# Optimization experiments

Measured on AMD Instinct MI355X. Metric: run time of the kernel, lower is better.

The kernel has to match this reference:

```python
import jax, jax.numpy as jnp
import numpy as np

INPUT_SIZE = 608
STRIDE = 32
NUM_CLASSES = 20
NMS_THRESH = 0.5
NUM_ANCHOR = 5
ANCHORS = np.array([[1.19, 1.98], [2.79, 4.59], [4.53, 8.92], [8.06, 5.29], [10.32, 10.65]], dtype=np.float32)


def _conv(x, w, b, pad):
    # x: NCHW, w: OIHW
    y = jax.lax.conv_general_dilated(x, w, (1, 1), [(pad, pad), (pad, pad)],
                                     dimension_numbers=('NCHW', 'OIHW', 'NCHW'))
    return y + b[None, :, None, None]


def _leaky(x):
    return jnp.where(x > 0, x, 0.1 * x)


def _reorg(x, s=2):
    # space-to-depth, darknet reorg: [B,C,H,W] -> [B,C*s*s,H/s,W/s]
    B, C, H, W = x.shape
    x = x.reshape(B, C, H // s, s, W // s, s)
    x = x.transpose(0, 3, 5, 1, 2, 4)
    return x.reshape(B, C * s * s, H // s, W // s)


def _forward_boxes_scores(feat_layer2, feat_layer3, w1a, b1a, w1b, b1b, wr, br, w2, b2, wp, bp):
    p5 = _leaky(_conv(feat_layer3, w1a, b1a, 1))
    p5 = _leaky(_conv(p5, w1b, b1b, 1))
    p4 = _reorg(_leaky(_conv(feat_layer2, wr, br, 0)))         # [1,256,19,19]
    p5 = jnp.concatenate([p4, p5], axis=1)                      # [1,1280,19,19]
    p5 = _leaky(_conv(p5, w2, b2, 1))
    pred = _conv(p5, wp, bp, 0)                                 # [1,125,19,19]
    B, C, H, W = pred.shape
    pred = pred.transpose(0, 2, 3, 1).reshape(B, H * W, C)
    conf = pred[:, :, :NUM_ANCHOR].reshape(B, H * W * NUM_ANCHOR, 1)
    cls = pred[:, :, NUM_ANCHOR:(1 + NUM_CLASSES) * NUM_ANCHOR].reshape(B, H * W * NUM_ANCHOR, NUM_CLASSES)
    reg = pred[:, :, (1 + NUM_CLASSES) * NUM_ANCHOR:].reshape(B, H * W, NUM_ANCHOR, 4)
    # decode_xywh
    gy, gx = jnp.meshgrid(jnp.arange(H), jnp.arange(W), indexing='ij')
    grid = jnp.stack([gx, gy], axis=-1).astype(pred.dtype).reshape(1, H * W, 1, 2)
    anchor_wh = jnp.asarray(ANCHORS).reshape(1, 1, NUM_ANCHOR, 2)
    xy = jax.nn.sigmoid(reg[..., :2]) + grid
    wh = jnp.exp(reg[..., 2:]) * anchor_wh
    xywh = jnp.concatenate([xy, wh], axis=-1).reshape(B, -1, 4) * STRIDE
    boxes = jnp.concatenate([xywh[..., :2] - 0.5 * xywh[..., 2:],
                             xywh[..., :2] + 0.5 * xywh[..., 2:]], axis=-1)
    boxes = jnp.clip(boxes[0] / INPUT_SIZE, 0.0, 1.0)           # [N,4]
    scores = jax.nn.sigmoid(conf[0]) * jax.nn.softmax(cls[0], axis=-1)  # [N,20]
    return boxes, scores


def _per_class_nms(boxes, scores, class_mask):
    # greedy sequential NMS, faithful to the torch while-loop (suppress iff IoU > thresh)
    N = boxes.shape[0]
    s = jnp.where(class_mask, scores, -jnp.inf)
    order = jnp.argsort(-s)
    b = boxes[order]
    valid = class_mask[order]
    x1, y1, x2, y2 = b[:, 0], b[:, 1], b[:, 2], b[:, 3]
    areas = (x2 - x1) * (y2 - y1)
    iw = jnp.maximum(1e-10, jnp.minimum(x2[:, None], x2[None, :]) - jnp.maximum(x1[:, None], x1[None, :]))
    ih = jnp.maximum(1e-10, jnp.minimum(y2[:, None], y2[None, :]) - jnp.maximum(y1[:, None], y1[None, :]))
    inter = iw * ih
    iou = inter / (areas[:, None] + areas[None, :] - inter)
    upper = jnp.arange(N)[None, :] > jnp.arange(N)[:, None]
    sup_mat = (iou > NMS_THRESH) & upper

    def body(i, state):
        suppressed, keep = state
        cur = valid[i] & jnp.logical_not(suppressed[i])
        keep = keep.at[i].set(cur)
        suppressed = suppressed | (cur & sup_mat[i])
        return suppressed, keep

    _, keep_sorted = jax.lax.fori_loop(0, N, body, (jnp.zeros(N, bool), jnp.zeros(N, bool)))
    return jnp.zeros(N, bool).at[order].set(keep_sorted)


def setup_inputs() -> dict:
    key = jax.random.key(0)
    ks = jax.random.split(key, 8)
    w = lambda k, shape: jax.random.normal(k, shape, jnp.float32) * 0.01
    return {
        'feat_layer2': jax.random.normal(ks[0], (1, 512, 38, 38), jnp.float32),
        'feat_layer3': jax.random.normal(ks[1], (1, 1024, 19, 19), jnp.float32),
        'w1a': w(ks[2], (1024, 1024, 3, 3)), 'b1a': jnp.zeros((1024,), jnp.float32),
        'w1b': w(ks[3], (1024, 1024, 3, 3)), 'b1b': jnp.zeros((1024,), jnp.float32),
        'wr': w(ks[4], (64, 512, 1, 1)), 'br': jnp.zeros((64,), jnp.float32),
        'w2': w(ks[5], (1024, 1280, 3, 3)), 'b2': jnp.zeros((1024,), jnp.float32),
        'wp': w(ks[6], (125, 1024, 1, 1)), 'bp': jnp.zeros((125,), jnp.float32),
    }


def reference(feat_layer2, feat_layer3, w1a, b1a, w1b, b1b, wr, br, w2, b2, wp, bp):
    boxes, scores_full = _forward_boxes_scores(feat_layer2, feat_layer3,
                                               w1a, b1a, w1b, b1b, wr, br, w2, b2, wp, bp)
    cls_inds = jnp.argmax(scores_full, axis=1)                          # [N]
    scores = jnp.take_along_axis(scores_full, cls_inds[:, None], axis=1)[:, 0]
    masks = cls_inds[None, :] == jnp.arange(NUM_CLASSES)[:, None]       # [20,N]
    keeps = jax.vmap(lambda m: _per_class_nms(boxes, scores, m))(masks)
    keep = jnp.any(keeps, axis=0)                                       # [N] bool, fixed-shape mask
    return boxes, scores, cls_inds, keep
```

## Files before the change

### kernel.cpp

```cpp
#include <hip/hip_runtime.h>

typedef _Float16 f16;
typedef _Float16 f16x8 __attribute__((ext_vector_type(8)));
typedef float f32x4 __attribute__((ext_vector_type(4)));

#define N_BOX 1805
#define NPIX 361
#define NCLS 20
#define GNW 29
#define MB_ROWS 226

__device__ __forceinline__ float leakyf(float x){ return x > 0.f ? x : 0.1f*x; }
__device__ __forceinline__ float sigmoidf_(float x){ return 1.f/(1.f + expf(-x)); }

__global__ void transpose_k(const float* __restrict__ src, float* __restrict__ dst, int R, int C){
  int i = blockIdx.x*256 + threadIdx.x;
  if (i < R*C){ int r = i / C, c = i % C; dst[c*R + r] = src[i]; }
}

__global__ void wprep_k(const float* __restrict__ w, f16* __restrict__ whi, f16* __restrict__ wlo,
                        int Cin, int total){
  int i = blockIdx.x*256 + threadIdx.x;
  if (i >= total) return;
  int co = i / Cin, ci = i - co*Cin;
  const float* src = w + (size_t)i*9;
  int K9 = 9*Cin;
  size_t dbase = (size_t)co*K9 + ci;
  #pragma unroll
  for (int t = 0; t < 9; ++t){
    float v = src[t]*64.f;
    f16 hi = (f16)v;
    f16 lo = (f16)(v - (float)hi);
    whi[dbase + (size_t)t*Cin] = hi;
    wlo[dbase + (size_t)t*Cin] = lo;
  }
}

__global__ void act1prep_k(const float* __restrict__ feat3, f16* __restrict__ ah, f16* __restrict__ al){
  int i = blockIdx.x*256 + threadIdx.x;
  if (i >= NPIX*1024) return;
  int p = i >> 10, c = i & 1023;
  float v = feat3[c*NPIX + p];
  f16 hi = (f16)v; f16 lo = (f16)(v - (float)hi);
  ah[i] = hi; al[i] = lo;
}

__global__ __launch_bounds__(256) void reorg_conv_k(const float* __restrict__ feat2,
    const float* __restrict__ wrT, const float* __restrict__ br,
    f16* __restrict__ cath, f16* __restrict__ catl){
  int c  = threadIdx.x & 63;
  int pq = threadIdx.x >> 6;
  int pix = blockIdx.x*4 + pq;
  int y = pix / 38, x = pix % 38;
  __shared__ float s_in[64][4];
  float acc = br[c];
  for (int cb = 0; cb < 512; cb += 64){
    __syncthreads();
    { int k = threadIdx.x >> 2, pp = threadIdx.x & 3;
      s_in[k][pp] = feat2[(cb + k)*1444 + blockIdx.x*4 + pp]; }
    __syncthreads();
    #pragma unroll
    for (int k = 0; k < 64; ++k)
      acc = fmaf(wrT[(cb+k)*64 + c], s_in[k][pq], acc);
  }
  float v = leakyf(acc);
  int co = ((y & 1)*2 + (x & 1))*64 + c;
  int p = (y>>1)*19 + (x>>1);
  f16 hi = (f16)v; f16 lo = (f16)(v - (float)hi);
  size_t o = (size_t)p*1280 + co;
  cath[o] = hi; catl[o] = lo;
}

__global__ __launch_bounds__(256) void conv_mfma_k(
    const f16* __restrict__ whi, const f16* __restrict__ wlo,
    const f16* __restrict__ ahi, const f16* __restrict__ alo,
    float* __restrict__ part, int Cin, int chunks, int cpt)
{
  const int K9 = 9*Cin;
  int cob = blockIdx.x * 128;
  int px0 = blockIdx.y * 128;
  int ks  = blockIdx.z;
  int kc0 = ks * chunks;
  int tid = threadIdx.x;

  __shared__ f16 sA[2][128*64];
  __shared__ f16 sB[2][128*64];

  int r = tid >> 1, h = tid & 1;
  int wboff[4];
  #pragma unroll
  for (int j = 0; j < 4; ++j)
    wboff[j] = (r*128 + (h*4 + j)*16) ^ ((r & 7) << 4);

  const f16* wArow = (h ? wlo : whi) + (size_t)(cob + r)*K9;
  int p = px0 + r;
  int py = p / 19, px = p - py*19;
  const f16* bbase = (h ? alo : ahi);

  int lane = tid & 63, wid = tid >> 6;
  int lrow = lane & 15, lgrp = lane >> 4;
  int wr = wid >> 1, wc = wid & 1;
  int aoffH[4], aoffL[4], boffH[4], boffL[4];
  #pragma unroll
  for (int m = 0; m < 4; ++m){
    int rA = wr*64 + m*16 + lrow;
    aoffH[m] = (rA*128 + lgrp*16)     ^ ((rA & 7) << 4);
    aoffL[m] = (rA*128 + (4+lgrp)*16) ^ ((rA & 7) << 4);
    int rB = wc*64 + m*16 + lrow;
    boffH[m] = (rB*128 + lgrp*16)     ^ ((rB & 7) << 4);
    boffL[m] = (rB*128 + (4+lgrp)*16) ^ ((rB & 7) << 4);
  }

  f32x4 acc[4][4] = {};
  f16x8 sa0, sa1, sa2, sa3, sb0, sb1, sb2, sb3;

  auto LOADK = [&](int kc){
    const f16* as = wArow + (size_t)kc*32;
    sa0 = *(const f16x8*)(as);
    sa1 = *(const f16x8*)(as + 8);
    sa2 = *(const f16x8*)(as + 16);
    sa3 = *(const f16x8*)(as + 24);
    int t = kc / cpt;
    int ci0 = (kc - t*cpt) * 32;
    int dy = t/3, dx = t - dy*3;
    int yy = py + dy - 1, xx = px + dx - 1;
    bool bvalid = (p < NPIX) && ((unsigned)yy < 19u) && ((unsigned)xx < 19u);
    f16x8 z = {};
    sb0 = z; sb1 = z; sb2 = z; sb3 = z;
    if (bvalid){
      const f16* bs = bbase + (size_t)(yy*19+xx)*Cin + ci0;
      sb0 = *(const f16x8*)(bs);
      sb1 = *(const f16x8*)(bs + 8);
      sb2 = *(const f16x8*)(bs + 16);
      sb3 = *(const f16x8*)(bs + 24);
    }
  };
  auto WRITEK = [&](int buf){
    *(f16x8*)((char*)sA[buf] + wboff[0]) = sa0;
    *(f16x8*)((char*)sA[buf] + wboff[1]) = sa1;
    *(f16x8*)((char*)sA[buf] + wboff[2]) = sa2;
    *(f16x8*)((char*)sA[buf] + wboff[3]) = sa3;
    *(f16x8*)((char*)sB[buf] + wboff[0]) = sb0;
    *(f16x8*)((char*)sB[buf] + wboff[1]) = sb1;
    *(f16x8*)((char*)sB[buf] + wboff[2]) = sb2;
    *(f16x8*)((char*)sB[buf] + wboff[3]) = sb3;
  };

  LOADK(kc0);
  WRITEK(0);
  __syncthreads();

  for (int i = 0; i < chunks; ++i){
    int cur = i & 1;
    bool more = (i + 1 < chunks);
    if (more) LOADK(kc0 + i + 1);

    f16x8 bh[4], bl[4];
    #pragma unroll
    for (int n = 0; n < 4; ++n){
      bh[n] = *(const f16x8*)((char*)sB[cur] + boffH[n]);
      bl[n] = *(const f16x8*)((char*)sB[cur] + boffL[n]);
    }
    #pragma unroll
    for (int m = 0; m < 4; ++m){
      f16x8 ah = *(const f16x8*)((char*)sA[cur] + aoffH[m]);
      f16x8 al = *(const f16x8*)((char*)sA[cur] + aoffL[m]);
      #pragma unroll
      for (int n = 0; n < 4; ++n){
        acc[m][n] = __builtin_amdgcn_mfma_f32_16x16x32_f16(ah, bh[n], acc[m][n], 0,0,0);
        acc[m][n] = __builtin_amdgcn_mfma_f32_16x16x32_f16(ah, bl[n], acc[m][n], 0,0,0);
        acc[m][n] = __builtin_amdgcn_mfma_f32_16x16x32_f16(al, bh[n], acc[m][n], 0,0,0);
      }
    }
    if (more) WRITEK(cur ^ 1);
    __syncthreads();
  }

  #pragma unroll
  for (int m = 0; m < 4; ++m){
    #pragma unroll
    for (int n = 0; n < 4; ++n){
      int pp = px0 + wc*64 + n*16 + lrow;
      if (pp < NPIX){
        int co = cob + wr*64 + m*16 + lgrp*4;
        size_t base = ((size_t)ks*1024 + co)*NPIX + pp;
        part[base          ] = acc[m][n][0];
        part[base +   NPIX ] = acc[m][n][1];
        part[base + 2*NPIX ] = acc[m][n][2];
        part[base + 3*NPIX ] = acc[m][n][3];
      }
    }
  }
}

__global__ void reduce16v_k(const float* __restrict__ part, const float* __restrict__ bias,
                            f16* __restrict__ dhi, f16* __restrict__ dlo,
                            int Cstride, int Coff, int splitk){
  int i = blockIdx.x*256 + threadIdx.x;
  if (i >= 1024*NPIX) return;
  int co = i / NPIX, p = i - co*NPIX;
  float s = 0.f;
  for (int k = 0; k < splitk; ++k) s += part[(size_t)k*1024*NPIX + i];
  float v = leakyf(s*0.015625f + bias[co]);
  f16 hi = (f16)v;
  f16 lo = (f16)(v - (float)hi);
  size_t o = (size_t)p*Cstride + Coff + co;
  dhi[o] = hi; dlo[o] = lo;
}

__global__ __launch_bounds__(256) void pred_conv_k(const f16* __restrict__ a3h, const f16* __restrict__ a3l,
    const float* __restrict__ wpT, const float* __restrict__ bp, float* __restrict__ pred){
  int c = threadIdx.x & 127, ph = threadIdx.x >> 7;
  int pix = blockIdx.x*2 + ph;
  __shared__ float s_in[64][2];
  float acc = 0.f;
  for (int cb = 0; cb < 1024; cb += 64){
    __syncthreads();
    if (threadIdx.x < 128){
      int k = threadIdx.x & 63, pp = threadIdx.x >> 6;
      int px2 = blockIdx.x*2 + pp;
      float v = 0.f;
      if (px2 < NPIX){
        size_t o = (size_t)px2*1024 + cb + k;
        v = (float)a3h[o] + (float)a3l[o];
      }
      s_in[k][pp] = v;
    }
    __syncthreads();
    if (c < 125){
      #pragma unroll
      for (int k = 0; k < 64; ++k)
        acc = fmaf(wpT[(cb+k)*125 + c], s_in[k][ph], acc);
    }
  }
  if (c < 125 && pix < NPIX) pred[c*NPIX + pix] = acc + bp[c];
}

__device__ const float ANCW[5] = {1.19f, 2.79f, 4.53f, 8.06f, 10.32f};
__device__ const float ANCH_[5] = {1.98f, 4.59f, 8.92f, 5.29f, 10.65f};

__global__ void decode_k(const float* __restrict__ pred, float* __restrict__ out,
                         int* __restrict__ cls_i, int* __restrict__ cnt){
  int n = blockIdx.x*256 + threadIdx.x;
  if (blockIdx.x == 0 && threadIdx.x < NCLS) cnt[threadIdx.x] = 0;
  if (n >= N_BOX) return;
  int p = n / 5, a = n % 5;
  float conf = pred[a*NPIX + p];
  float cl[20]; float m = -1e30f;
  #pragma unroll
  for (int k = 0; k < 20; ++k){ cl[k] = pred[(5 + a*20 + k)*NPIX + p]; m = fmaxf(m, cl[k]); }
  float s = 0.f;
  #pragma unroll
  for (int k = 0; k < 20; ++k){ cl[k] = expf(cl[k]-m); s += cl[k]; }
  int bi = 0; float bv = cl[0];
  #pragma unroll
  for (int k = 1; k < 20; ++k) if (cl[k] > bv){ bv = cl[k]; bi = k; }
  float score = sigmoidf_(conf) * (bv / s);
  float tx = pred[(105 + a*4 + 0)*NPIX + p];
  float ty = pred[(105 + a*4 + 1)*NPIX + p];
  float tw = pred[(105 + a*4 + 2)*NPIX + p];
  float th = pred[(105 + a*4 + 3)*NPIX + p];
  float gx = (float)(p % 19), gy = (float)(p / 19);
  float cx = (sigmoidf_(tx) + gx) * 32.f;
  float cy = (sigmoidf_(ty) + gy) * 32.f;
  float bw = expf(tw) * ANCW[a] * 32.f;
  float bh = expf(th) * ANCH_[a] * 32.f;
  float x1 = fminf(fmaxf((cx - 0.5f*bw) / 608.f, 0.f), 1.f);
  float y1 = fminf(fmaxf((cy - 0.5f*bh) / 608.f, 0.f), 1.f);
  float x2 = fminf(fmaxf((cx + 0.5f*bw) / 608.f, 0.f), 1.f);
  float y2 = fminf(fmaxf((cy + 0.5f*bh) / 608.f, 0.f), 1.f);
  out[n*4+0]=x1; out[n*4+1]=y1; out[n*4+2]=x2; out[n*4+3]=y2;
  out[7220 + n]  = score;
  out[9025 + n]  = (float)bi;
  out[10830 + n] = 0.f;
  cls_i[n] = bi;
}

__global__ __launch_bounds__(256) void rank_k(const float* __restrict__ scores,
    const int* __restrict__ cls_i, int* __restrict__ ord, int* __restrict__ cnt){
  __shared__ float s_sc[N_BOX];
  __shared__ short s_cl[N_BOX];
  int tid = threadIdx.x;
  for (int j = tid; j < N_BOX; j += 256){ s_sc[j] = scores[j]; s_cl[j] = (short)cls_i[j]; }
  __syncthreads();
  int wid = tid >> 6, lane = tid & 63;
  int i = blockIdx.x*4 + wid;
  if (i >= N_BOX) return;
  float si = s_sc[i]; short ci = s_cl[i];
  int r = 0;
  for (int j = lane; j < N_BOX; j += 64){
    float sj = s_sc[j];
    r += (int)((s_cl[j] == ci) & ((sj > si) | ((sj == si) & (j < i))));
  }
  #pragma unroll
  for (int o = 32; o; o >>= 1) r += __shfl_down(r, o);
  if (lane == 0){
    ord[ci*N_BOX + r] = i;
    atomicAdd(&cnt[ci], 1);
  }
}

__global__ __launch_bounds__(256) void maskbuild_k(const float* __restrict__ boxes,
    const int* __restrict__ ord, const int* __restrict__ cnt,
    unsigned long long* __restrict__ gmask){
  __shared__ float X1[N_BOX], Y1[N_BOX], X2[N_BOX], Y2[N_BOX], AR[N_BOX];
  int c = blockIdx.x, chunk = blockIdx.y, tid = threadIdx.x;
  int n = cnt[c];
  int r0 = chunk*MB_ROWS;
  if (n <= 0 || r0 >= n) return;
  int r1 = r0 + MB_ROWS; if (r1 > n) r1 = n;
  int rows_here = r1 - r0;
  for (int t = tid; t < n; t += 256){
    int bi = ord[c*N_BOX + t];
    float x1 = boxes[bi*4+0], y1 = boxes[bi*4+1], x2 = boxes[bi*4+2], y2 = boxes[bi*4+3];
    X1[t]=x1; Y1[t]=y1; X2[t]=x2; Y2[t]=y2; AR[t]=(x2-x1)*(y2-y1);
  }
  __syncthreads();
  int nw = (n + 63) >> 6;
  unsigned long long* rows = gmask + (size_t)c*N_BOX*GNW;
  for (int task = tid; task < rows_here*nw; task += 256){
    int w = task / rows_here, ri = task - w*rows_here;
    int i = r0 + ri;
    float ax1=X1[i], ay1=Y1[i], ax2=X2[i], ay2=Y2[i], areaA=AR[i];
    unsigned long long bits = 0;
    int j0 = w << 6;
    int jb = i+1 > j0 ? i+1 : j0;
    int je = j0+64 < n ? j0+64 : n;
    for (int j = jb; j < je; ++j){
      float iw = fmaxf(1e-10f, fminf(ax2,X2[j]) - fmaxf(ax1,X1[j]));
      float ih = fmaxf(1e-10f, fminf(ay2,Y2[j]) - fmaxf(ay1,Y1[j]));
      float inter = iw*ih;
      float iou = inter / (areaA + AR[j] - inter);
      bits |= (unsigned long long)(iou > 0.5f) << (j - j0);
    }
    rows[(size_t)i*GNW + w] = bits;
  }
}

__global__ __launch_bounds__(64) void nmsscan_k(const int* __restrict__ ord,
    const int* __restrict__ cnt, const unsigned long long* __restrict__ gmask,
    float* __restrict__ keep){
  __shared__ int sidx[N_BOX];
  int c = blockIdx.x, lane = threadIdx.x;
  int n = cnt[c];
  if (n <= 0) return;
  int nw = (n + 63) >> 6;
  for (int t = lane; t < n; t += 64) sidx[t] = ord[c*N_BOX + t];
  __syncthreads();
  const unsigned long long* rows = gmask + (size_t)c*N_BOX*GNW;
  bool act = lane < nw;
  unsigned long long S = 0;
  unsigned long long diag = (lane < n) ? rows[(size_t)lane*GNW + 0] : 0ull;
  for (int w = 0; w < nw; ++w){
    int base = w << 6;
    int nb = n - base; if (nb > 64) nb = 64;
    unsigned int slo = (unsigned)__builtin_amdgcn_readlane((int)(unsigned)S, w);
    unsigned int shi = (unsigned)__builtin_amdgcn_readlane((int)(unsigned)(S >> 32), w);
    unsigned long long sup = ((unsigned long long)shi << 32) | slo;
    unsigned long long validm = (nb >= 64) ? ~0ull : ((1ull << nb) - 1ull);
    unsigned long long avail = ~sup & validm;
    unsigned long long kmask = 0;
    unsigned long long diag_next = 0;
    if (w+1 < nw){
      int i2 = base + 64 + lane;
      if (i2 < n) diag_next = rows[(size_t)i2*GNW + (w+1)];
    }
    while (avail){
      int b = __builtin_ctzll(avail);
      kmask |= 1ull << b;
      unsigned int dlo = (unsigned)__builtin_amdgcn_readlane((int)(unsigned)diag, b);
      unsigned int dhi = (unsigned)__builtin_amdgcn_readlane((int)(unsigned)(diag >> 32), b);
      unsigned long long drow = ((unsigned long long)dhi << 32) | dlo;
      sup |= drow;
      avail &= ~(1ull << b);
      avail &= ~sup;
      if (act && lane > w)
        S |= rows[(size_t)(base + b)*GNW + lane];
    }
    if ((kmask >> lane) & 1ull) keep[sidx[base + lane]] = 1.f;
    diag = diag_next;
  }
}

static inline size_t align256(size_t x){ return (x + 255) & ~(size_t)255; }

extern "C" void kernel_launch(void* const* d_in, const int* in_sizes, int n_in,
                              void* d_out, int out_size, void* d_ws, size_t ws_size,
                              hipStream_t stream){
  const float* feat2 = (const float*)d_in[0];
  const float* feat3 = (const float*)d_in[1];
  const float* w1a = (const float*)d_in[2];
  const float* b1a = (const float*)d_in[3];
  const float* w1b = (const float*)d_in[4];
  const float* b1b = (const float*)d_in[5];
  const float* wr  = (const float*)d_in[6];
  const float* br  = (const float*)d_in[7];
  const float* w2  = (const float*)d_in[8];
  const float* b2  = (const float*)d_in[9];
  const float* wp  = (const float*)d_in[10];
  const float* bp  = (const float*)d_in[11];
  float* out = (float*)d_out;
  char* ws = (char*)d_ws;

  size_t off = 0;
  float* part = (float*)(ws + off); off = align256(off + (size_t)24*1024*NPIX*4);
  f16* wh   = (f16*)(ws + off); off = align256(off + (size_t)1024*1280*9*2);
  f16* wl   = (f16*)(ws + off); off = align256(off + (size_t)1024*1280*9*2);
  f16* a1h  = (f16*)(ws + off); off = align256(off + (size_t)NPIX*1024*2);
  f16* a1l  = (f16*)(ws + off); off = align256(off + (size_t)NPIX*1024*2);
  f16* a2h  = (f16*)(ws + off); off = align256(off + (size_t)NPIX*1024*2);
  f16* a2l  = (f16*)(ws + off); off = align256(off + (size_t)NPIX*1024*2);
  f16* a3h  = (f16*)(ws + off); off = align256(off + (size_t)NPIX*1024*2);
  f16* a3l  = (f16*)(ws + off); off = align256(off + (size_t)NPIX*1024*2);
  f16* cath = (f16*)(ws + off); off = align256(off + (size_t)NPIX*1280*2);
  f16* catl = (f16*)(ws + off); off = align256(off + (size_t)NPIX*1280*2);
  float* pred = (float*)(ws + off); off = align256(off + (size_t)125*NPIX*4);
  float* wrT  = (float*)(ws + off); off = align256(off + (size_t)512*64*4);
  float* wpT  = (float*)(ws + off); off = align256(off + (size_t)1024*125*4);
  int* cls_i  = (int*)(ws + off); off = align256(off + (size_t)N_BOX*4);
  int* ord    = (int*)(ws + off); off = align256(off + (size_t)NCLS*N_BOX*4);
  int* cnt    = (int*)(ws + off); off = align256(off + (size_t)NCLS*4);
  unsigned long long* gmask = (unsigned long long*)part;

  transpose_k<<<(64*512 + 255)/256, 256, 0, stream>>>(wr, wrT, 64, 512);
  transpose_k<<<(125*1024 + 255)/256, 256, 0, stream>>>(wp, wpT, 125, 1024);
  act1prep_k<<<(NPIX*1024 + 255)/256, 256, 0, stream>>>(feat3, a1h, a1l);
  reorg_conv_k<<<361, 256, 0, stream>>>(feat2, wrT, br, cath, catl);

  wprep_k<<<(1024*1024 + 255)/256, 256, 0, stream>>>(w1a, wh, wl, 1024, 1024*1024);
  { dim3 g(8, 3, 24);
    conv_mfma_k<<<g, 256, 0, stream>>>(wh, wl, a1h, a1l, part, 1024, 12, 32); }
  reduce16v_k<<<(1024*NPIX + 255)/256, 256, 0, stream>>>(part, b1a, a2h, a2l, 1024, 0, 24);

  wprep_k<<<(1024*1024 + 255)/256, 256, 0, stream>>>(w1b, wh, wl, 1024, 1024*1024);
  { dim3 g(8, 3, 24);
    conv_mfma_k<<<g, 256, 0, stream>>>(wh, wl, a2h, a2l, part, 1024, 12, 32); }
  reduce16v_k<<<(1024*NPIX + 255)/256, 256, 0, stream>>>(part, b1b, cath, catl, 1280, 256, 24);

  wprep_k<<<(1024*1280 + 255)/256, 256, 0, stream>>>(w2, wh, wl, 1280, 1024*1280);
  { dim3 g(8, 3, 24);
    conv_mfma_k<<<g, 256, 0, stream>>>(wh, wl, cath, catl, part, 1280, 15, 40); }
  reduce16v_k<<<(1024*NPIX + 255)/256, 256, 0, stream>>>(part, b2, a3h, a3l, 1024, 0, 24);

  pred_conv_k<<<181, 256, 0, stream>>>(a3h, a3l, wpT, bp, pred);
  decode_k<<<8, 256, 0, stream>>>(pred, out, cls_i, cnt);
  rank_k<<<(N_BOX + 3)/4, 256, 0, stream>>>(out + 7220, cls_i, ord, cnt);
  { dim3 mg(NCLS, 8);
    maskbuild_k<<<mg, 256, 0, stream>>>(out, ord, cnt, gmask); }
  nmsscan_k<<<NCLS, 64, 0, stream>>>(ord, cnt, gmask, out + 10830);
}
```

Before: 350.2 us.

## Pre-pack conv weights into swizzled LDS-tile order and reduce split-K

Weight prep now writes hi/lo f16 halves into per-tile packed blocks already in the swizzled shared-memory layout, so the conv kernel loads each A tile with fully contiguous 16-byte accesses and copies it straight to LDS. The split-K factor drops from 24 to 16/18, giving longer K loops per block and fewer partial sums to write and reduce. The trade-off is fewer blocks in flight (384/432 instead of 576) and a more complex prep kernel with strided reads from the original weights.

```diff
diff --git a/kernel.cpp b/kernel.cpp
--- a/kernel.cpp
+++ b/kernel.cpp
@@ -18,22 +18,29 @@
   if (i < R*C){ int r = i / C, c = i % C; dst[c*R + r] = src[i]; }
 }
 
-__global__ void wprep_k(const float* __restrict__ w, f16* __restrict__ whi, f16* __restrict__ wlo,
-                        int Cin, int total){
-  int i = blockIdx.x*256 + threadIdx.x;
-  if (i >= total) return;
-  int co = i / Cin, ci = i - co*Cin;
-  const float* src = w + (size_t)i*9;
-  int K9 = 9*Cin;
-  size_t dbase = (size_t)co*K9 + ci;
-  #pragma unroll
-  for (int t = 0; t < 9; ++t){
-    float v = src[t]*64.f;
+__global__ void wprep_packed_k(const float* __restrict__ w, f16* __restrict__ wpk,
+                               int Cin, int cpt, int NK){
+  int gid = blockIdx.x*256 + threadIdx.x;
+  if (gid >= 8*NK*1024) return;
+  int g    = gid & 1023;
+  int tile = gid >> 10;
+  int kc   = tile % NK;
+  int cob  = tile / NK;
+  int row  = g >> 3, sraw = g & 7;
+  int sdata = sraw ^ (row & 7);
+  int h = sdata >> 2, jci = sdata & 3;
+  int t = kc / cpt;
+  int ci0 = (kc - t*cpt)*32 + jci*8;
+  int co = cob*128 + row;
+  const float* src = w + ((size_t)co*Cin + ci0)*9 + t;
+  f16x8 outv;
+  #pragma unroll
+  for (int k = 0; k < 8; ++k){
+    float v = src[(size_t)k*9] * 64.f;
     f16 hi = (f16)v;
-    f16 lo = (f16)(v - (float)hi);
-    whi[dbase + (size_t)t*Cin] = hi;
-    wlo[dbase + (size_t)t*Cin] = lo;
-  }
+    outv[k] = h ? (f16)(v - (float)hi) : hi;
+  }
+  *(f16x8*)(wpk + (size_t)tile*8192 + g*8) = outv;
 }
 
 __global__ void act1prep_k(const float* __restrict__ feat3, f16* __restrict__ ah, f16* __restrict__ al){
@@ -72,12 +79,11 @@
 }
 
 __global__ __launch_bounds__(256) void conv_mfma_k(
-    const f16* __restrict__ whi, const f16* __restrict__ wlo,
+    const f16* __restrict__ wpk,
     const f16* __restrict__ ahi, const f16* __restrict__ alo,
-    float* __restrict__ part, int Cin, int chunks, int cpt)
+    float* __restrict__ part, int Cin, int chunks, int cpt, int NK)
 {
-  const int K9 = 9*Cin;
-  int cob = blockIdx.x * 128;
+  int cob = blockIdx.x;
   int px0 = blockIdx.y * 128;
   int ks  = blockIdx.z;
   int kc0 = ks * chunks;
@@ -86,13 +92,16 @@
   __shared__ f16 sA[2][128*64];
   __shared__ f16 sB[2][128*64];
 
+  const f16* wbase = wpk + ((size_t)cob*NK + kc0)*8192;
+  int aost[4];
+  #pragma unroll
+  for (int j = 0; j < 4; ++j) aost[j] = (tid + j*256)*8;
+
   int r = tid >> 1, h = tid & 1;
   int wboff[4];
   #pragma unroll
   for (int j = 0; j < 4; ++j)
     wboff[j] = (r*128 + (h*4 + j)*16) ^ ((r & 7) << 4);
-
-  const f16* wArow = (h ? wlo : whi) + (size_t)(cob + r)*K9;
   int p = px0 + r;
   int py = p / 19, px = p - py*19;
   const f16* bbase = (h ? alo : ahi);
@@ -114,12 +123,13 @@
   f32x4 acc[4][4] = {};
   f16x8 sa0, sa1, sa2, sa3, sb0, sb1, sb2, sb3;
 
-  auto LOADK = [&](int kc){
-    const f16* as = wArow + (size_t)kc*32;
-    sa0 = *(const f16x8*)(as);
-    sa1 = *(const f16x8*)(as + 8);
-    sa2 = *(const f16x8*)(as + 16);
-    sa3 = *(const f16x8*)(as + 24);
+  auto LOADK = [&](int i){
+    const f16* as = wbase + (size_t)i*8192;
+    sa0 = *(const f16x8*)(as + aost[0]);
+    sa1 = *(const f16x8*)(as + aost[1]);
+    sa2 = *(const f16x8*)(as + aost[2]);
+    sa3 = *(const f16x8*)(as + aost[3]);
+    int kc = kc0 + i;
     int t = kc / cpt;
     int ci0 = (kc - t*cpt) * 32;
     int dy = t/3, dx = t - dy*3;
@@ -136,24 +146,24 @@
     }
   };
   auto WRITEK = [&](int buf){
-    *(f16x8*)((char*)sA[buf] + wboff[0]) = sa0;
-    *(f16x8*)((char*)sA[buf] + wboff[1]) = sa1;
-    *(f16x8*)((char*)sA[buf] + wboff[2]) = sa2;
-    *(f16x8*)((char*)sA[buf] + wboff[3]) = sa3;
+    *(f16x8*)(&sA[buf][aost[0]]) = sa0;
+    *(f16x8*)(&sA[buf][aost[1]]) = sa1;
+    *(f16x8*)(&sA[buf][aost[2]]) = sa2;
+    *(f16x8*)(&sA[buf][aost[3]]) = sa3;
     *(f16x8*)((char*)sB[buf] + wboff[0]) = sb0;
     *(f16x8*)((char*)sB[buf] + wboff[1]) = sb1;
     *(f16x8*)((char*)sB[buf] + wboff[2]) = sb2;
     *(f16x8*)((char*)sB[buf] + wboff[3]) = sb3;
   };
 
-  LOADK(kc0);
+  LOADK(0);
   WRITEK(0);
   __syncthreads();
 
   for (int i = 0; i < chunks; ++i){
     int cur = i & 1;
     bool more = (i + 1 < chunks);
-    if (more) LOADK(kc0 + i + 1);
+    if (more) LOADK(i + 1);
 
     f16x8 bh[4], bl[4];
     #pragma unroll
@@ -182,7 +192,7 @@
     for (int n = 0; n < 4; ++n){
       int pp = px0 + wc*64 + n*16 + lrow;
       if (pp < NPIX){
-        int co = cob + wr*64 + m*16 + lgrp*4;
+        int co = cob*128 + wr*64 + m*16 + lgrp*4;
         size_t base = ((size_t)ks*1024 + co)*NPIX + pp;
         part[base          ] = acc[m][n][0];
         part[base +   NPIX ] = acc[m][n][1];
@@ -404,8 +414,7 @@
 
   size_t off = 0;
   float* part = (float*)(ws + off); off = align256(off + (size_t)24*1024*NPIX*4);
-  f16* wh   = (f16*)(ws + off); off = align256(off + (size_t)1024*1280*9*2);
-  f16* wl   = (f16*)(ws + off); off = align256(off + (size_t)1024*1280*9*2);
+  f16* wpk  = (f16*)(ws + off); off = align256(off + (size_t)8*360*8192*2);
   f16* a1h  = (f16*)(ws + off); off = align256(off + (size_t)NPIX*1024*2);
   f16* a1l  = (f16*)(ws + off); off = align256(off + (size_t)NPIX*1024*2);
   f16* a2h  = (f16*)(ws + off); off = align256(off + (size_t)NPIX*1024*2);
@@ -427,20 +436,20 @@
   act1prep_k<<<(NPIX*1024 + 255)/256, 256, 0, stream>>>(feat3, a1h, a1l);
   reorg_conv_k<<<361, 256, 0, stream>>>(feat2, wrT, br, cath, catl);
 
-  wprep_k<<<(1024*1024 + 255)/256, 256, 0, stream>>>(w1a, wh, wl, 1024, 1024*1024);
-  { dim3 g(8, 3, 24);
-    conv_mfma_k<<<g, 256, 0, stream>>>(wh, wl, a1h, a1l, part, 1024, 12, 32); }
-  reduce16v_k<<<(1024*NPIX + 255)/256, 256, 0, stream>>>(part, b1a, a2h, a2l, 1024, 0, 24);
-
-  wprep_k<<<(1024*1024 + 255)/256, 256, 0, stream>>>(w1b, wh, wl, 1024, 1024*1024);
-  { dim3 g(8, 3, 24);
-    conv_mfma_k<<<g, 256, 0, stream>>>(wh, wl, a2h, a2l, part, 1024, 12, 32); }
-  reduce16v_k<<<(1024*NPIX + 255)/256, 256, 0, stream>>>(part, b1b, cath, catl, 1280, 256, 24);
-
-  wprep_k<<<(1024*1280 + 255)/256, 256, 0, stream>>>(w2, wh, wl, 1280, 1024*1280);
-  { dim3 g(8, 3, 24);
-    conv_mfma_k<<<g, 256, 0, stream>>>(wh, wl, cath, catl, part, 1280, 15, 40); }
-  reduce16v_k<<<(1024*NPIX + 255)/256, 256, 0, stream>>>(part, b2, a3h, a3l, 1024, 0, 24);
+  wprep_packed_k<<<(8*288*1024)/256, 256, 0, stream>>>(w1a, wpk, 1024, 32, 288);
+  { dim3 g(8, 3, 16);
+    conv_mfma_k<<<g, 256, 0, stream>>>(wpk, a1h, a1l, part, 1024, 18, 32, 288); }
+  reduce16v_k<<<(1024*NPIX + 255)/256, 256, 0, stream>>>(part, b1a, a2h, a2l, 1024, 0, 16);
+
+  wprep_packed_k<<<(8*288*1024)/256, 256, 0, stream>>>(w1b, wpk, 1024, 32, 288);
+  { dim3 g(8, 3, 16);
+    conv_mfma_k<<<g, 256, 0, stream>>>(wpk, a2h, a2l, part, 1024, 18, 32, 288); }
+  reduce16v_k<<<(1024*NPIX + 255)/256, 256, 0, stream>>>(part, b1b, cath, catl, 1280, 256, 16);
+
+  wprep_packed_k<<<(8*360*1024)/256, 256, 0, stream>>>(w2, wpk, 1280, 40, 360);
+  { dim3 g(8, 3, 18);
+    conv_mfma_k<<<g, 256, 0, stream>>>(wpk, cath, catl, part, 1280, 20, 40, 360); }
+  reduce16v_k<<<(1024*NPIX + 255)/256, 256, 0, stream>>>(part, b2, a3h, a3l, 1024, 0, 18);
 
   pred_conv_k<<<181, 256, 0, stream>>>(a3h, a3l, wpT, bp, pred);
   decode_k<<<8, 256, 0, stream>>>(pred, out, cls_i, cnt);
```

Result: faster. 321.7 us (-8.1%).
